# Kernel tuning notes

Measured on AMD Instinct MI355X. Metric: run time of the kernel, lower is better.

The kernel has to match this reference:

```python
import jax, jax.numpy as jnp
import numpy as np


def setup_inputs() -> dict:
    key = jax.random.key(0)
    ks = jax.random.split(key, 8)
    B, C, H, W = 4, 256, 64, 64
    x = jax.random.normal(ks[0], (B, C, H, W), dtype=jnp.float32)
    y = jax.random.normal(ks[1], (B, C, H, W), dtype=jnp.float32)
    s = 1.0 / np.sqrt(C)
    Wq = jax.random.normal(ks[2], (C, C), dtype=jnp.float32) * s
    bq = jax.random.normal(ks[3], (C,), dtype=jnp.float32) * 0.02
    Wk = jax.random.normal(ks[4], (C, C), dtype=jnp.float32) * s
    bk = jax.random.normal(ks[5], (C,), dtype=jnp.float32) * 0.02
    Wv = jax.random.normal(ks[6], (C, C), dtype=jnp.float32) * s
    bv = jax.random.normal(ks[7], (C,), dtype=jnp.float32) * 0.02
    return {"x": x, "y": y, "Wq": Wq, "bq": bq, "Wk": Wk, "bk": bk, "Wv": Wv, "bv": bv}


def reference(x, y, Wq, bq, Wk, bk, Wv, bv):
    B, C, H, W = x.shape
    scale = C ** (-0.5)
    # flatten spatial dims: [B, N, C] with N = H*W
    x_flat = x.reshape(B, C, H * W).transpose(0, 2, 1)
    y_flat = y.reshape(B, C, H * W).transpose(0, 2, 1)
    # linear projections (torch Linear: x @ W.T + b)
    Q = jnp.einsum('bnc,dc->bnd', x_flat, Wq) + bq
    K = jnp.einsum('bnc,dc->bnd', y_flat, Wk) + bk
    V = jnp.einsum('bnc,dc->bnd', y_flat, Wv) + bv
    # single-head full cross-attention
    scores = jnp.einsum('bqd,bkd->bqk', Q, K) * scale  # [B, N, N]
    attn = jax.nn.softmax(scores, axis=-1)
    out = jnp.einsum('bqk,bkd->bqd', attn, V)  # [B, N, C]
    out = out.transpose(0, 2, 1).reshape(B, C, H, W)
    return x + out
```

## Files before the change

### kernel.cpp

```cpp
#include <hip/hip_runtime.h>
#include <stdint.h>

#define BN 4
#define CD 256
#define ND 4096
#define NK 32

typedef unsigned short u16;
typedef short bfrag __attribute__((ext_vector_type(8)));
typedef float ffrag __attribute__((ext_vector_type(4)));

__device__ __forceinline__ float bf2f(u16 u) {
  union { unsigned int i; float f; } v;
  v.i = ((unsigned int)u) << 16;
  return v.f;
}
__device__ __forceinline__ u16 f2bf(float f) {
  union { float f; unsigned int i; } v;
  v.f = f;
  return (u16)((v.i + 0x7FFFu + ((v.i >> 16) & 1u)) >> 16);
}
__device__ __forceinline__ void gload_lds(const u16* g, u16* l) {
  __builtin_amdgcn_global_load_lds(
      (const __attribute__((address_space(1))) void*)g,
      (__attribute__((address_space(3))) void*)l, 16, 0, 0);
}

__global__ __launch_bounds__(256, 2) void k_projQK(
    const float* __restrict__ x, const float* __restrict__ y,
    const float* __restrict__ Wq, const float* __restrict__ Wk,
    const float* __restrict__ bq, const float* __restrict__ bk,
    u16* __restrict__ Qb, u16* __restrict__ Kb) {
  __shared__ alignas(16) u16 As[64][264];
  __shared__ alignas(16) u16 Bs[64][136];
  int n0 = blockIdx.x * 64;
  int m0 = blockIdx.y * 64;
  int z = blockIdx.z;
  int b = m0 >> 12, nsp = m0 & 4095;
  const float* src = (z ? y : x) + (size_t)b * CD * ND;
  const float* Wsrc = (z ? Wk : Wq) + (size_t)n0 * CD;
  const float* bias = (z ? bk : bq) + n0;
  u16* Cd = (z ? Kb : Qb) + (size_t)m0 * CD + n0;
  int t = threadIdx.x, w = t >> 6, l = t & 63;
  int lane16 = l & 15, quad = l >> 4;

#pragma unroll
  for (int it = 0; it < 16; ++it) {
    int idx = it * 256 + t;
    int c = idx >> 4, nj = (idx & 15) * 4;
    float4 v = *(const float4*)(src + (size_t)c * ND + nsp + nj);
    As[nj + 0][c] = f2bf(v.x);
    As[nj + 1][c] = f2bf(v.y);
    As[nj + 2][c] = f2bf(v.z);
    As[nj + 3][c] = f2bf(v.w);
  }

  ffrag acc[4];
#pragma unroll
  for (int tt = 0; tt < 4; ++tt) acc[tt] = ffrag{0.f, 0.f, 0.f, 0.f};
#pragma unroll
  for (int half = 0; half < 2; ++half) {
    if (half) __syncthreads();
#pragma unroll
    for (int it = 0; it < 8; ++it) {
      int idx = it * 256 + t;
      int row = idx >> 5, cj = (idx & 31) * 4;
      float4 v = *(const float4*)(Wsrc + (size_t)row * CD + half * 128 + cj);
      ushort4 o;
      o.x = f2bf(v.x); o.y = f2bf(v.y); o.z = f2bf(v.z); o.w = f2bf(v.w);
      *(ushort4*)&Bs[row][cj] = o;
    }
    __syncthreads();
#pragma unroll
    for (int kc = 0; kc < 4; ++kc) {
      bfrag af = *(const bfrag*)&As[w * 16 + lane16][half * 128 + kc * 32 + quad * 8];
#pragma unroll
      for (int tt = 0; tt < 4; ++tt) {
        bfrag bfr = *(const bfrag*)&Bs[tt * 16 + lane16][kc * 32 + quad * 8];
        acc[tt] = __builtin_amdgcn_mfma_f32_16x16x32_bf16(af, bfr, acc[tt], 0, 0, 0);
      }
    }
  }
#pragma unroll
  for (int tt = 0; tt < 4; ++tt) {
    int colL = tt * 16 + lane16;
    float bcol = bias[colL];
#pragma unroll
    for (int r = 0; r < 4; ++r) {
      int rowL = w * 16 + quad * 4 + r;
      Cd[(size_t)rowL * CD + colL] = f2bf(acc[tt][r] + bcol);
    }
  }
}

__global__ __launch_bounds__(256, 2) void k_projV(
    const float* __restrict__ y, const float* __restrict__ Wv,
    const float* __restrict__ bv, u16* __restrict__ Vb) {
  __shared__ alignas(16) u16 As[64][264];
  __shared__ alignas(16) u16 Bs[64][136];
  int n0s = blockIdx.x * 64;
  int m0 = blockIdx.y * 64;
  int b = blockIdx.z;
  const float* Bsrc = y + (size_t)b * CD * ND + n0s;
  u16* Cd = Vb + ((size_t)b * CD + m0) * ND + n0s;
  int t = threadIdx.x, w = t >> 6, l = t & 63;
  int lane16 = l & 15, quad = l >> 4;

#pragma unroll
  for (int it = 0; it < 16; ++it) {
    int idx = it * 256 + t;
    int row = idx >> 6, cj = (idx & 63) * 4;
    float4 v = *(const float4*)(Wv + (size_t)(m0 + row) * CD + cj);
    ushort4 o;
    o.x = f2bf(v.x); o.y = f2bf(v.y); o.z = f2bf(v.z); o.w = f2bf(v.w);
    *(ushort4*)&As[row][cj] = o;
  }

  ffrag acc[4];
#pragma unroll
  for (int tt = 0; tt < 4; ++tt) acc[tt] = ffrag{0.f, 0.f, 0.f, 0.f};
#pragma unroll
  for (int half = 0; half < 2; ++half) {
    if (half) __syncthreads();
#pragma unroll
    for (int it = 0; it < 8; ++it) {
      int idx = it * 256 + t;
      int cl = idx >> 4, nj = (idx & 15) * 4;
      float4 v = *(const float4*)(Bsrc + (size_t)(half * 128 + cl) * ND + nj);
      Bs[nj + 0][cl] = f2bf(v.x);
      Bs[nj + 1][cl] = f2bf(v.y);
      Bs[nj + 2][cl] = f2bf(v.z);
      Bs[nj + 3][cl] = f2bf(v.w);
    }
    __syncthreads();
#pragma unroll
    for (int kc = 0; kc < 4; ++kc) {
      bfrag af = *(const bfrag*)&As[w * 16 + lane16][half * 128 + kc * 32 + quad * 8];
#pragma unroll
      for (int tt = 0; tt < 4; ++tt) {
        bfrag bfr = *(const bfrag*)&Bs[tt * 16 + lane16][kc * 32 + quad * 8];
        acc[tt] = __builtin_amdgcn_mfma_f32_16x16x32_bf16(af, bfr, acc[tt], 0, 0, 0);
      }
    }
  }
#pragma unroll
  for (int tt = 0; tt < 4; ++tt) {
    int colL = tt * 16 + lane16;
#pragma unroll
    for (int r = 0; r < 4; ++r) {
      int rowL = w * 16 + quad * 4 + r;
      Cd[(size_t)rowL * ND + colL] = f2bf(acc[tt][r] + bv[m0 + rowL]);
    }
  }
}

union SmemU {
  struct {
    u16 Ks[2][NK][256];
    u16 Vs[2][CD][NK];
    u16 Ps[8][16][40];
  } a;
  u16 ot[CD][136];
};

template <int NS>
__global__ __launch_bounds__(256, 2) void k_attn(
    const u16* __restrict__ Q, const u16* __restrict__ K,
    const u16* __restrict__ Vt, u16* __restrict__ O01,
    u16* __restrict__ O23, float* __restrict__ Lpart) {
  constexpr int NIT = ND / NS / NK;
  __shared__ alignas(16) SmemU sm;
  int b = blockIdx.y, q0 = blockIdx.x * 128, z = blockIdx.z;
  int t = threadIdx.x, w = t >> 6, l = t & 63;
  int lane16 = l & 15, quad = l >> 4;
  const float scale = 0.0625f;

  bfrag qf[2][8];
#pragma unroll
  for (int mi = 0; mi < 2; ++mi) {
    const u16* Qrow =
        Q + ((size_t)b * ND + q0 + (w * 2 + mi) * 16 + lane16) * CD;
#pragma unroll
    for (int kc = 0; kc < 8; ++kc)
      qf[mi][kc] = *(const bfrag*)(Qrow + kc * 32 + quad * 8);
  }

  ffrag o[2][16];
#pragma unroll
  for (int mi = 0; mi < 2; ++mi)
#pragma unroll
    for (int i = 0; i < 16; ++i) o[mi][i] = ffrag{0.f, 0.f, 0.f, 0.f};
  float lsum[2][4] = {{0.f, 0.f, 0.f, 0.f}, {0.f, 0.f, 0.f, 0.f}};

  const u16* Kb = K + ((size_t)b * ND + z * (ND / NS)) * CD;
  const u16* Vb = Vt + (size_t)b * CD * ND + z * (ND / NS);

  auto stage = [&](int kt2) {
    int dbuf = kt2 & 1;
    const u16* Kt = Kb + (size_t)kt2 * NK * CD;
    const u16* Vtt = Vb + kt2 * NK;
#pragma unroll
    for (int p = 0; p < 4; ++p) {
      int r = p * 8 + w * 2 + (l >> 5);
      int j = (l & 31) ^ (r & 7);
      gload_lds(Kt + (size_t)r * CD + j * 8, &sm.a.Ks[dbuf][p * 8 + w * 2][0]);
    }
#pragma unroll
    for (int p = 0; p < 4; ++p) {
      int dd = p * 64 + w * 16 + (l >> 2);
      int j = (l & 3) ^ ((dd >> 1) & 3);
      gload_lds(Vtt + (size_t)dd * ND + j * 8, &sm.a.Vs[dbuf][p * 64 + w * 16][0]);
    }
  };

  stage(0);
  for (int kt = 0; kt < NIT; ++kt) {
    int dbuf = kt & 1;
    __syncthreads();
    if (kt + 1 < NIT) stage(kt + 1);

    ffrag s2[2][2];
#pragma unroll
    for (int mi = 0; mi < 2; ++mi)
#pragma unroll
      for (int tt = 0; tt < 2; ++tt) s2[mi][tt] = ffrag{0.f, 0.f, 0.f, 0.f};
#pragma unroll
    for (int kc = 0; kc < 8; ++kc) {
      bfrag kf0, kf1;
      {
        int r = lane16;
        int cp = (kc * 4 + quad) ^ (r & 7);
        kf0 = *(const bfrag*)&sm.a.Ks[dbuf][r][cp * 8];
        int r1 = 16 + lane16;
        int cp1 = (kc * 4 + quad) ^ (r1 & 7);
        kf1 = *(const bfrag*)&sm.a.Ks[dbuf][r1][cp1 * 8];
      }
#pragma unroll
      for (int mi = 0; mi < 2; ++mi) {
        s2[mi][0] = __builtin_amdgcn_mfma_f32_16x16x32_bf16(qf[mi][kc], kf0,
                                                            s2[mi][0], 0, 0, 0);
        s2[mi][1] = __builtin_amdgcn_mfma_f32_16x16x32_bf16(qf[mi][kc], kf1,
                                                            s2[mi][1], 0, 0, 0);
      }
    }

#pragma unroll
    for (int mi = 0; mi < 2; ++mi)
#pragma unroll
      for (int tt = 0; tt < 2; ++tt)
#pragma unroll
        for (int r = 0; r < 4; ++r) {
          float p = __expf(s2[mi][tt][r] * scale);
          lsum[mi][r] += p;
          sm.a.Ps[w * 2 + mi][quad * 4 + r][tt * 16 + lane16] = f2bf(p);
        }
    bfrag pf0 = *(const bfrag*)&sm.a.Ps[w * 2 + 0][lane16][quad * 8];
    bfrag pf1 = *(const bfrag*)&sm.a.Ps[w * 2 + 1][lane16][quad * 8];

#pragma unroll
    for (int dt = 0; dt < 16; ++dt) {
      int dd = dt * 16 + lane16;
      int cp = quad ^ ((dd >> 1) & 3);
      bfrag vf = *(const bfrag*)&sm.a.Vs[dbuf][dd][cp * 8];
      o[0][dt] = __builtin_amdgcn_mfma_f32_16x16x32_bf16(pf0, vf, o[0][dt], 0, 0, 0);
      o[1][dt] = __builtin_amdgcn_mfma_f32_16x16x32_bf16(pf1, vf, o[1][dt], 0, 0, 0);
    }
  }

#pragma unroll
  for (int mi = 0; mi < 2; ++mi)
#pragma unroll
    for (int r = 0; r < 4; ++r) {
#pragma unroll
      for (int off = 1; off < 16; off <<= 1)
        lsum[mi][r] += __shfl_xor(lsum[mi][r], off, 64);
    }
  if (lane16 == 0) {
#pragma unroll
    for (int mi = 0; mi < 2; ++mi)
#pragma unroll
      for (int r = 0; r < 4; ++r)
        Lpart[((size_t)z * BN + b) * ND + q0 + (w * 2 + mi) * 16 + quad * 4 + r] =
            lsum[mi][r];
  }

  __syncthreads();
#pragma unroll
  for (int mi = 0; mi < 2; ++mi)
#pragma unroll
    for (int dt = 0; dt < 16; ++dt)
#pragma unroll
      for (int r = 0; r < 4; ++r)
        sm.ot[dt * 16 + lane16][(w * 2 + mi) * 16 + quad * 4 + r] =
            f2bf(o[mi][dt][r]);
  __syncthreads();
  const size_t SZc = (size_t)BN * ND * CD;
  u16* Op = ((z < 2) ? O01 : O23) + (size_t)(z & 1) * SZc;
#pragma unroll
  for (int it = 0; it < 16; ++it) {
    int c = it * 256 + t;
    int dd = c >> 4, co = (c & 15) * 8;
    size_t g = ((size_t)b * CD + dd) * ND + q0 + co;
    *(uint4*)(Op + g) = *(const uint4*)&sm.ot[dd][co];
  }
}

template <int NS>
__global__ __launch_bounds__(256) void k_combine(
    const u16* __restrict__ O01, const u16* __restrict__ O23,
    const float* __restrict__ L, const float* __restrict__ x,
    float* __restrict__ out) {
  const size_t SZc = (size_t)BN * ND * CD;
  size_t e = ((size_t)blockIdx.x * 256 + threadIdx.x) * 8;
  int n = (int)(e & (ND - 1));
  int b = (int)(e >> 20);
  float ls[8] = {0, 0, 0, 0, 0, 0, 0, 0};
  float acc[8] = {0, 0, 0, 0, 0, 0, 0, 0};
#pragma unroll
  for (int z = 0; z < NS; ++z) {
    const float* Lr = L + ((size_t)z * BN + b) * ND + n;
    float4 l0 = *(const float4*)(Lr);
    float4 l1 = *(const float4*)(Lr + 4);
    ls[0] += l0.x; ls[1] += l0.y; ls[2] += l0.z; ls[3] += l0.w;
    ls[4] += l1.x; ls[5] += l1.y; ls[6] += l1.z; ls[7] += l1.w;
    const u16* Oz = ((z < 2) ? O01 : O23) + (size_t)(z & 1) * SZc + e;
    union { uint4 q; u16 s[8]; } u;
    u.q = *(const uint4*)Oz;
#pragma unroll
    for (int j = 0; j < 8; ++j) acc[j] += bf2f(u.s[j]);
  }
  float4 x0 = *(const float4*)(x + e);
  float4 x1 = *(const float4*)(x + e + 4);
  float4 r0, r1;
  r0.x = x0.x + acc[0] / ls[0];
  r0.y = x0.y + acc[1] / ls[1];
  r0.z = x0.z + acc[2] / ls[2];
  r0.w = x0.w + acc[3] / ls[3];
  r1.x = x1.x + acc[4] / ls[4];
  r1.y = x1.y + acc[5] / ls[5];
  r1.z = x1.z + acc[6] / ls[6];
  r1.w = x1.w + acc[7] / ls[7];
  *(float4*)(out + e) = r0;
  *(float4*)(out + e + 4) = r1;
}

extern "C" void kernel_launch(void* const* d_in, const int* in_sizes, int n_in,
                              void* d_out, int out_size, void* d_ws, size_t ws_size,
                              hipStream_t stream) {
  const float* x  = (const float*)d_in[0];
  const float* y  = (const float*)d_in[1];
  const float* Wq = (const float*)d_in[2];
  const float* bq = (const float*)d_in[3];
  const float* Wk = (const float*)d_in[4];
  const float* bk = (const float*)d_in[5];
  const float* Wv = (const float*)d_in[6];
  const float* bv = (const float*)d_in[7];
  float* out = (float*)d_out;
  u16* ws = (u16*)d_ws;
  const size_t SZ = (size_t)BN * ND * CD;
  u16* Qb = ws;
  u16* Kb = Qb + SZ;
  u16* Vb = Kb + SZ;
  u16* Ob = Vb + SZ;
  const size_t need4 = 7 * SZ * sizeof(u16) + (size_t)4 * BN * ND * sizeof(float);
  const bool big = ws_size >= need4;
  const int cgrid = (int)(SZ / (256 * 8));

  k_projQK<<<dim3(4, 256, 2), 256, 0, stream>>>(x, y, Wq, Wk, bq, bk, Qb, Kb);
  k_projV<<<dim3(64, 4, 4), 256, 0, stream>>>(y, Wv, bv, Vb);
  if (big) {
    float* Lp = (float*)(Ob + 4 * SZ);
    k_attn<4><<<dim3(ND / 128, BN, 4), 256, 0, stream>>>(Qb, Kb, Vb, Ob,
                                                         Ob + 2 * SZ, Lp);
    k_combine<4><<<dim3(cgrid), 256, 0, stream>>>(Ob, Ob + 2 * SZ, Lp, x, out);
  } else {
    float* Lp = (float*)(Ob + 2 * SZ);
    k_attn<2><<<dim3(ND / 128, BN, 2), 256, 0, stream>>>(Qb, Kb, Vb, Ob, Ob, Lp);
    k_combine<2><<<dim3(cgrid), 256, 0, stream>>>(Ob, Ob, Lp, x, out);
  }
}
```

Baseline: 211.8 us.

## Pre-convert weights to bf16 and compute full-width projection tiles per block

Adds a small kernel that converts Wq, Wk and Wv to bf16 once into workspace. The projection kernels then have each block compute all 256 output channels for a 64-row activation tile, reading the bf16 weights directly from global memory (L2-cached) rather than staging them in LDS. This removes the repeated activation-tile loading and fp32-to-bf16 conversion across output-column blocks, and cuts the grid size by 4x. The cost is higher register use (16 accumulators plus 8 fragments per thread), uncoalesced global weight fragment reads, and one extra launch.

Result: slower. 232.2 us (+9.6%).

```diff
diff --git a/kernel.cpp b/kernel.cpp
--- a/kernel.cpp
+++ b/kernel.cpp
@@ -26,21 +26,31 @@
       (__attribute__((address_space(3))) void*)l, 16, 0, 0);
 }
 
+__global__ __launch_bounds__(256) void k_cvtW(
+    const float* __restrict__ Wq, const float* __restrict__ Wk,
+    const float* __restrict__ Wv, u16* __restrict__ wb) {
+  int m = blockIdx.y;
+  const float* src = (m == 0) ? Wq : ((m == 1) ? Wk : Wv);
+  u16* dst = wb + (size_t)m * CD * CD;
+  int i = (blockIdx.x * 256 + threadIdx.x) * 4;
+  float4 v = *(const float4*)(src + i);
+  ushort4 o;
+  o.x = f2bf(v.x); o.y = f2bf(v.y); o.z = f2bf(v.z); o.w = f2bf(v.w);
+  *(ushort4*)(dst + i) = o;
+}
+
 __global__ __launch_bounds__(256, 2) void k_projQK(
     const float* __restrict__ x, const float* __restrict__ y,
-    const float* __restrict__ Wq, const float* __restrict__ Wk,
-    const float* __restrict__ bq, const float* __restrict__ bk,
-    u16* __restrict__ Qb, u16* __restrict__ Kb) {
+    const u16* __restrict__ wB, const float* __restrict__ bq,
+    const float* __restrict__ bk, u16* __restrict__ Qb, u16* __restrict__ Kb) {
   __shared__ alignas(16) u16 As[64][264];
-  __shared__ alignas(16) u16 Bs[64][136];
-  int n0 = blockIdx.x * 64;
-  int m0 = blockIdx.y * 64;
-  int z = blockIdx.z;
+  int m0 = blockIdx.x * 64;
+  int z = blockIdx.y;
   int b = m0 >> 12, nsp = m0 & 4095;
   const float* src = (z ? y : x) + (size_t)b * CD * ND;
-  const float* Wsrc = (z ? Wk : Wq) + (size_t)n0 * CD;
-  const float* bias = (z ? bk : bq) + n0;
-  u16* Cd = (z ? Kb : Qb) + (size_t)m0 * CD + n0;
+  const u16* Wsrc = wB + (size_t)z * CD * CD;
+  const float* bias = z ? bk : bq;
+  u16* Cd = (z ? Kb : Qb) + (size_t)m0 * CD;
   int t = threadIdx.x, w = t >> 6, l = t & 63;
   int lane16 = l & 15, quad = l >> 4;
 
@@ -54,102 +64,83 @@
     As[nj + 2][c] = f2bf(v.z);
     As[nj + 3][c] = f2bf(v.w);
   }
-
-  ffrag acc[4];
-#pragma unroll
-  for (int tt = 0; tt < 4; ++tt) acc[tt] = ffrag{0.f, 0.f, 0.f, 0.f};
-#pragma unroll
-  for (int half = 0; half < 2; ++half) {
-    if (half) __syncthreads();
-#pragma unroll
-    for (int it = 0; it < 8; ++it) {
-      int idx = it * 256 + t;
-      int row = idx >> 5, cj = (idx & 31) * 4;
-      float4 v = *(const float4*)(Wsrc + (size_t)row * CD + half * 128 + cj);
-      ushort4 o;
-      o.x = f2bf(v.x); o.y = f2bf(v.y); o.z = f2bf(v.z); o.w = f2bf(v.w);
-      *(ushort4*)&Bs[row][cj] = o;
-    }
-    __syncthreads();
-#pragma unroll
-    for (int kc = 0; kc < 4; ++kc) {
-      bfrag af = *(const bfrag*)&As[w * 16 + lane16][half * 128 + kc * 32 + quad * 8];
-#pragma unroll
-      for (int tt = 0; tt < 4; ++tt) {
-        bfrag bfr = *(const bfrag*)&Bs[tt * 16 + lane16][kc * 32 + quad * 8];
-        acc[tt] = __builtin_amdgcn_mfma_f32_16x16x32_bf16(af, bfr, acc[tt], 0, 0, 0);
-      }
-    }
-  }
-#pragma unroll
-  for (int tt = 0; tt < 4; ++tt) {
-    int colL = tt * 16 + lane16;
-    float bcol = bias[colL];
+  __syncthreads();
+
+  bfrag af[8];
+#pragma unroll
+  for (int kc = 0; kc < 8; ++kc)
+    af[kc] = *(const bfrag*)&As[w * 16 + lane16][kc * 32 + quad * 8];
+
+  ffrag acc[16];
+#pragma unroll
+  for (int i = 0; i < 16; ++i) acc[i] = ffrag{0.f, 0.f, 0.f, 0.f};
+#pragma unroll
+  for (int kc = 0; kc < 8; ++kc) {
+#pragma unroll
+    for (int nt = 0; nt < 16; ++nt) {
+      bfrag bfr = *(const bfrag*)(Wsrc + (size_t)(nt * 16 + lane16) * CD +
+                                  kc * 32 + quad * 8);
+      acc[nt] = __builtin_amdgcn_mfma_f32_16x16x32_bf16(af[kc], bfr, acc[nt], 0, 0, 0);
+    }
+  }
+#pragma unroll
+  for (int nt = 0; nt < 16; ++nt) {
+    int col = nt * 16 + lane16;
+    float bcol = bias[col];
 #pragma unroll
     for (int r = 0; r < 4; ++r) {
       int rowL = w * 16 + quad * 4 + r;
-      Cd[(size_t)rowL * CD + colL] = f2bf(acc[tt][r] + bcol);
+      Cd[(size_t)rowL * CD + col] = f2bf(acc[nt][r] + bcol);
     }
   }
 }
 
 __global__ __launch_bounds__(256, 2) void k_projV(
-    const float* __restrict__ y, const float* __restrict__ Wv,
+    const float* __restrict__ y, const u16* __restrict__ WvB,
     const float* __restrict__ bv, u16* __restrict__ Vb) {
-  __shared__ alignas(16) u16 As[64][264];
-  __shared__ alignas(16) u16 Bs[64][136];
+  __shared__ alignas(16) u16 Bs[64][264];
   int n0s = blockIdx.x * 64;
-  int m0 = blockIdx.y * 64;
-  int b = blockIdx.z;
-  const float* Bsrc = y + (size_t)b * CD * ND + n0s;
-  u16* Cd = Vb + ((size_t)b * CD + m0) * ND + n0s;
+  int b = blockIdx.y;
+  const float* src = y + (size_t)b * CD * ND;
+  u16* Cd = Vb + (size_t)b * CD * ND;
   int t = threadIdx.x, w = t >> 6, l = t & 63;
   int lane16 = l & 15, quad = l >> 4;
 
 #pragma unroll
   for (int it = 0; it < 16; ++it) {
     int idx = it * 256 + t;
-    int row = idx >> 6, cj = (idx & 63) * 4;
-    float4 v = *(const float4*)(Wv + (size_t)(m0 + row) * CD + cj);
-    ushort4 o;
-    o.x = f2bf(v.x); o.y = f2bf(v.y); o.z = f2bf(v.z); o.w = f2bf(v.w);
-    *(ushort4*)&As[row][cj] = o;
-  }
-
-  ffrag acc[4];
-#pragma unroll
-  for (int tt = 0; tt < 4; ++tt) acc[tt] = ffrag{0.f, 0.f, 0.f, 0.f};
-#pragma unroll
-  for (int half = 0; half < 2; ++half) {
-    if (half) __syncthreads();
-#pragma unroll
-    for (int it = 0; it < 8; ++it) {
-      int idx = it * 256 + t;
-      int cl = idx >> 4, nj = (idx & 15) * 4;
-      float4 v = *(const float4*)(Bsrc + (size_t)(half * 128 + cl) * ND + nj);
-      Bs[nj + 0][cl] = f2bf(v.x);
-      Bs[nj + 1][cl] = f2bf(v.y);
-      Bs[nj + 2][cl] = f2bf(v.z);
-      Bs[nj + 3][cl] = f2bf(v.w);
-    }
-    __syncthreads();
-#pragma unroll
-    for (int kc = 0; kc < 4; ++kc) {
-      bfrag af = *(const bfrag*)&As[w * 16 + lane16][half * 128 + kc * 32 + quad * 8];
-#pragma unroll
-      for (int tt = 0; tt < 4; ++tt) {
-        bfrag bfr = *(const bfrag*)&Bs[tt * 16 + lane16][kc * 32 + quad * 8];
-        acc[tt] = __builtin_amdgcn_mfma_f32_16x16x32_bf16(af, bfr, acc[tt], 0, 0, 0);
-      }
-    }
-  }
-#pragma unroll
-  for (int tt = 0; tt < 4; ++tt) {
-    int colL = tt * 16 + lane16;
+    int c = idx >> 4, nj = (idx & 15) * 4;
+    float4 v = *(const float4*)(src + (size_t)c * ND + n0s + nj);
+    Bs[nj + 0][c] = f2bf(v.x);
+    Bs[nj + 1][c] = f2bf(v.y);
+    Bs[nj + 2][c] = f2bf(v.z);
+    Bs[nj + 3][c] = f2bf(v.w);
+  }
+  __syncthreads();
+
+  bfrag bfr[8];
+#pragma unroll
+  for (int kc = 0; kc < 8; ++kc)
+    bfr[kc] = *(const bfrag*)&Bs[w * 16 + lane16][kc * 32 + quad * 8];
+
+  ffrag o[16];
+#pragma unroll
+  for (int i = 0; i < 16; ++i) o[i] = ffrag{0.f, 0.f, 0.f, 0.f};
+#pragma unroll
+  for (int kc = 0; kc < 8; ++kc) {
+#pragma unroll
+    for (int mt = 0; mt < 16; ++mt) {
+      bfrag af = *(const bfrag*)(WvB + (size_t)(mt * 16 + lane16) * CD +
+                                 kc * 32 + quad * 8);
+      o[mt] = __builtin_amdgcn_mfma_f32_16x16x32_bf16(af, bfr[kc], o[mt], 0, 0, 0);
+    }
+  }
+#pragma unroll
+  for (int mt = 0; mt < 16; ++mt) {
 #pragma unroll
     for (int r = 0; r < 4; ++r) {
-      int rowL = w * 16 + quad * 4 + r;
-      Cd[(size_t)rowL * ND + colL] = f2bf(acc[tt][r] + bv[m0 + rowL]);
+      int d = mt * 16 + quad * 4 + r;
+      Cd[(size_t)d * ND + n0s + w * 16 + lane16] = f2bf(o[mt][r] + bv[d]);
     }
   }
 }
@@ -362,12 +353,14 @@
   u16* Kb = Qb + SZ;
   u16* Vb = Kb + SZ;
   u16* Ob = Vb + SZ;
+  u16* wB = Ob;
   const size_t need4 = 7 * SZ * sizeof(u16) + (size_t)4 * BN * ND * sizeof(float);
   const bool big = ws_size >= need4;
   const int cgrid = (int)(SZ / (256 * 8));
 
-  k_projQK<<<dim3(4, 256, 2), 256, 0, stream>>>(x, y, Wq, Wk, bq, bk, Qb, Kb);
-  k_projV<<<dim3(64, 4, 4), 256, 0, stream>>>(y, Wv, bv, Vb);
+  k_cvtW<<<dim3(64, 3), 256, 0, stream>>>(Wq, Wk, Wv, wB);
+  k_projQK<<<dim3(256, 2), 256, 0, stream>>>(x, y, wB, bq, bk, Qb, Kb);
+  k_projV<<<dim3(64, 4), 256, 0, stream>>>(y, wB + (size_t)2 * CD * CD, bv, Vb);
   if (big) {
     float* Lp = (float*)(Ob + 4 * SZ);
     k_attn<4><<<dim3(ND / 128, BN, 4), 256, 0, stream>>>(Qb, Kb, Vb, Ob,
```
